# Performance work log

Measured on AMD Instinct MI355X. Metric: run time of the kernel, lower is better.

Reference implementation:

```python
import jax, jax.numpy as jnp
import numpy as np

B, T, N, D = 32, 32, 64, 512
H, OUT = 64, 256


def setup_inputs() -> dict:
    key = jax.random.key(0)
    ks = jax.random.split(key, 7)
    return {
        "inputs": jax.random.normal(ks[0], (B, T, N, D), dtype=jnp.float32),
        "ue_w": jax.random.normal(ks[1], (H, D), dtype=jnp.float32) * (1.0 / np.sqrt(D)),
        "ue_b": jax.random.normal(ks[2], (H,), dtype=jnp.float32) * 0.02,
        "be": jnp.zeros((H,), dtype=jnp.float32),
        "w_w": jax.random.normal(ks[3], (1, H), dtype=jnp.float32) * (1.0 / np.sqrt(H)),
        "w_b": jax.random.normal(ks[4], (1,), dtype=jnp.float32) * 0.02,
        "fc1_w": jax.random.normal(ks[5], (OUT, D), dtype=jnp.float32) * (1.0 / np.sqrt(D)),
        "fc1_b": jax.random.normal(ks[6], (OUT,), dtype=jnp.float32) * 0.02,
    }


def reference(inputs, ue_w, ue_b, be, w_w, w_b, fc1_w, fc1_b):
    # Train path of STAttn.
    b, t, n, d = inputs.shape
    x = inputs.reshape(b * t, n, d)                       # flatten(start=0, end=1)
    h = jnp.einsum('bnd,hd->bnh', x, ue_w) + ue_b + be    # ue(x) + be
    h = jax.nn.leaky_relu(h, negative_slope=0.2)
    e = jnp.einsum('bnh,oh->bno', h, w_w) + w_b           # [BT, N, 1] scores
    a = jax.nn.softmax(e, axis=-2)                        # softmax over N
    attr = jnp.sum(a * x, axis=1)                         # weighted pooling -> [BT, D]
    fc = attr @ fc1_w.T + fc1_b                           # [BT, 256]
    return fc.reshape(b, t, fc.shape[-1]).transpose(1, 0, 2)  # [T, B, 256]
```

## Files before the change

### kernel.cpp

```cpp
#include <hip/hip_runtime.h>


typedef __attribute__((ext_vector_type(8)))  short bf16x8;
typedef __attribute__((ext_vector_type(16))) float f32x16;

#define SPL(f, i) do {                                                        \
    const unsigned u_ = __float_as_uint(f);                                   \
    h8[i] = (short)(u_ >> 16);                                                \
    const float hf_ = __uint_as_float(u_ & 0xFFFF0000u);                      \
    l8[i] = (short)(__float_as_uint((f) - hf_) >> 16);                        \
} while (0)

__device__ __forceinline__ void split8v(float4 va, float4 vb,
                                        bf16x8& h8, bf16x8& l8) {
    SPL(va.x, 0); SPL(va.y, 1); SPL(va.z, 2); SPL(va.w, 3);
    SPL(vb.x, 4); SPL(vb.y, 5); SPL(vb.z, 6); SPL(vb.w, 7);
}

template<int MODE>
__global__ __launch_bounds__(256, 2) void stattn_ea(
    const float* __restrict__ inp,
    const float* __restrict__ ue_w,
    const float* __restrict__ ue_b,
    const float* __restrict__ be,
    const float* __restrict__ w_w,
    const float* __restrict__ fc1_w,
    const float* __restrict__ fc1_b,
    float* __restrict__ dst)
{
    __shared__ float e_s[2][64];
    __shared__ float a_s[2][64];
    __shared__ __align__(16) float attr_s[2][512];

    const int tid = threadIdx.x;
    const int wv  = tid >> 6;
    const int l   = tid & 63;
    const int l31 = l & 31;
    const int hi5 = l >> 5;
    const int g   = wv >> 1;
    const int nh  = wv & 1;
    const long bt = (long)blockIdx.x * 2 + g;
    const float* __restrict__ xg = inp + bt * (64 * 512);

    const float* __restrict__ arow  = xg   + (nh * 32 + l31) * 512 + hi5 * 8;
    const float* __restrict__ brow0 = ue_w + l31 * 512 + hi5 * 8;
    const float* __restrict__ brow1 = brow0 + 32 * 512;

    f32x16 acc0 = {}, acc1 = {};
#pragma unroll 4
    for (int ks = 0; ks < 32; ++ks) {
        const int k = ks * 16;
        const float4 a0  = *reinterpret_cast<const float4*>(&arow[k]);
        const float4 a1  = *reinterpret_cast<const float4*>(&arow[k + 4]);
        const float4 b00 = *reinterpret_cast<const float4*>(&brow0[k]);
        const float4 b01 = *reinterpret_cast<const float4*>(&brow0[k + 4]);
        const float4 b10 = *reinterpret_cast<const float4*>(&brow1[k]);
        const float4 b11 = *reinterpret_cast<const float4*>(&brow1[k + 4]);
        bf16x8 ah, al, bh0, bl0, bh1, bl1;
        { bf16x8 &h8 = ah,  &l8 = al;  split8v(a0,  a1,  h8, l8); }
        { bf16x8 &h8 = bh0, &l8 = bl0; split8v(b00, b01, h8, l8); }
        { bf16x8 &h8 = bh1, &l8 = bl1; split8v(b10, b11, h8, l8); }
        acc0 = __builtin_amdgcn_mfma_f32_32x32x16_bf16(ah, bh0, acc0, 0, 0, 0);
        acc0 = __builtin_amdgcn_mfma_f32_32x32x16_bf16(al, bh0, acc0, 0, 0, 0);
        acc0 = __builtin_amdgcn_mfma_f32_32x32x16_bf16(ah, bl0, acc0, 0, 0, 0);
        acc1 = __builtin_amdgcn_mfma_f32_32x32x16_bf16(ah, bh1, acc1, 0, 0, 0);
        acc1 = __builtin_amdgcn_mfma_f32_32x32x16_bf16(al, bh1, acc1, 0, 0, 0);
        acc1 = __builtin_amdgcn_mfma_f32_32x32x16_bf16(ah, bl1, acc1, 0, 0, 0);
    }

    {
        const int j0 = l31, j1 = l31 + 32;
        const float bias0 = ue_b[j0] + be[j0];
        const float bias1 = ue_b[j1] + be[j1];
        const float ww0 = w_w[j0], ww1 = w_w[j1];
#pragma unroll
        for (int r = 0; r < 16; ++r) {
            float h0 = acc0[r] + bias0; h0 = h0 > 0.f ? h0 : 0.2f * h0;
            float h1 = acc1[r] + bias1; h1 = h1 > 0.f ? h1 : 0.2f * h1;
            float p = h0 * ww0 + h1 * ww1;
            p += __shfl_xor(p, 1);
            p += __shfl_xor(p, 2);
            p += __shfl_xor(p, 4);
            p += __shfl_xor(p, 8);
            p += __shfl_xor(p, 16);
            if (l31 == 0)
                e_s[g][nh * 32 + (r & 3) + 8 * (r >> 2) + 4 * hi5] = p;
        }
    }
    __syncthreads();

    {
        const float v = e_s[g][l];
        float mx = v;
#pragma unroll
        for (int off = 32; off >= 1; off >>= 1) mx = fmaxf(mx, __shfl_xor(mx, off));
        const float ex = expf(v - mx);
        float sm = ex;
#pragma unroll
        for (int off = 32; off >= 1; off >>= 1) sm += __shfl_xor(sm, off);
        a_s[g][l] = ex / sm;
    }
    __syncthreads();

    {
        const float* __restrict__ xp = xg + nh * 256 + 4 * l;
        float sx = 0.f, sy = 0.f, sz = 0.f, sw = 0.f;
#pragma unroll 8
        for (int n = 0; n < 64; ++n) {
            const float an  = a_s[g][n];
            const float4 xv = *reinterpret_cast<const float4*>(&xp[n * 512]);
            sx = fmaf(an, xv.x, sx);
            sy = fmaf(an, xv.y, sy);
            sz = fmaf(an, xv.z, sz);
            sw = fmaf(an, xv.w, sw);
        }
        float4 o; o.x = sx; o.y = sy; o.z = sz; o.w = sw;
        if (MODE == 0) {
            *reinterpret_cast<float4*>(&dst[bt * 512 + nh * 256 + 4 * l]) = o;
        } else {
            *reinterpret_cast<float4*>(&attr_s[g][nh * 256 + 4 * l]) = o;
        }
    }

    if (MODE == 1) {
        __syncthreads();
        const int o = tid;
#pragma unroll
        for (int gg = 0; gg < 2; ++gg) {
            const float* __restrict__ wr = fc1_w + o * 512;
            const float* __restrict__ ap = attr_s[gg];
            float s0 = 0.f, s1 = 0.f, s2 = 0.f, s3 = 0.f;
#pragma unroll 8
            for (int i = 0; i < 128; ++i) {
                const float4 w4 = *reinterpret_cast<const float4*>(&wr[i * 4]);
                const float4 a4 = *reinterpret_cast<const float4*>(&ap[i * 4]);
                s0 = fmaf(a4.x, w4.x, s0);
                s1 = fmaf(a4.y, w4.y, s1);
                s2 = fmaf(a4.z, w4.z, s2);
                s3 = fmaf(a4.w, w4.w, s3);
            }
            const long btg = (long)blockIdx.x * 2 + gg;
            const int row  = (int)(btg & 31) * 32 + (int)(btg >> 5);
            dst[row * 256 + o] = (s0 + s1) + (s2 + s3) + fc1_b[o];
        }
    }
}

__global__ __launch_bounds__(256, 2) void stattn_fc2(
    const float* __restrict__ attr,
    const float* __restrict__ fc1_w,
    const float* __restrict__ fc1_b,
    float* __restrict__ out)
{
    __shared__ __align__(16) float at[32][516];
    const int tid = threadIdx.x;
    const int bm  = blockIdx.x;
    const int bn  = blockIdx.y;

    {
        const int row = tid >> 3;
        const int seg = tid & 7;
        const float* __restrict__ src = attr + (size_t)(bm * 32 + row) * 512 + seg * 64;
#pragma unroll
        for (int q = 0; q < 16; ++q)
            *reinterpret_cast<float4*>(&at[row][seg * 64 + q * 4]) =
                *reinterpret_cast<const float4*>(&src[q * 4]);
    }
    __syncthreads();

    const int tx = tid & 31;
    const int ty = tid >> 5;
    const int o  = bn * 32 + tx;
    const float* __restrict__ wr = fc1_w + (size_t)o * 512;
    float s0 = 0.f, s1 = 0.f, s2 = 0.f, s3 = 0.f;
#pragma unroll 4
    for (int kq = 0; kq < 128; ++kq) {
        const float4 w4 = *reinterpret_cast<const float4*>(&wr[kq * 4]);
        const float4 a0 = *reinterpret_cast<const float4*>(&at[ty * 4 + 0][kq * 4]);
        const float4 a1 = *reinterpret_cast<const float4*>(&at[ty * 4 + 1][kq * 4]);
        const float4 a2 = *reinterpret_cast<const float4*>(&at[ty * 4 + 2][kq * 4]);
        const float4 a3 = *reinterpret_cast<const float4*>(&at[ty * 4 + 3][kq * 4]);
        s0 += a0.x * w4.x + a0.y * w4.y + a0.z * w4.z + a0.w * w4.w;
        s1 += a1.x * w4.x + a1.y * w4.y + a1.z * w4.z + a1.w * w4.w;
        s2 += a2.x * w4.x + a2.y * w4.y + a2.z * w4.z + a2.w * w4.w;
        s3 += a3.x * w4.x + a3.y * w4.y + a3.z * w4.z + a3.w * w4.w;
    }
    const float fb = fc1_b[o];
    float sv0 = s0 + fb, sv1 = s1 + fb, sv2 = s2 + fb, sv3 = s3 + fb;
    {
        int btv = bm * 32 + ty * 4;
        out[((btv & 31) * 32 + (btv >> 5)) * 256 + o] = sv0; ++btv;
        out[((btv & 31) * 32 + (btv >> 5)) * 256 + o] = sv1; ++btv;
        out[((btv & 31) * 32 + (btv >> 5)) * 256 + o] = sv2; ++btv;
        out[((btv & 31) * 32 + (btv >> 5)) * 256 + o] = sv3;
    }
}

extern "C" void kernel_launch(void* const* d_in, const int* in_sizes, int n_in,
                              void* d_out, int out_size, void* d_ws, size_t ws_size,
                              hipStream_t stream) {
    const float* inp   = (const float*)d_in[0];
    const float* ue_w  = (const float*)d_in[1];
    const float* ue_b  = (const float*)d_in[2];
    const float* be    = (const float*)d_in[3];
    const float* w_w   = (const float*)d_in[4];
    const float* fc1_w = (const float*)d_in[6];
    const float* fc1_b = (const float*)d_in[7];
    float* out = (float*)d_out;

    const bool split = ws_size >= (size_t)1024 * 512 * 4;
    if (split) {
        float* attr = (float*)d_ws;
        stattn_ea<0><<<512, 256, 0, stream>>>(inp, ue_w, ue_b, be, w_w,
                                              fc1_w, fc1_b, attr);
        stattn_fc2<<<dim3(32, 8), 256, 0, stream>>>(attr, fc1_w, fc1_b, out);
    } else {
        stattn_ea<1><<<512, 256, 0, stream>>>(inp, ue_w, ue_b, be, w_w,
                                              fc1_w, fc1_b, out);
    }
}
```

Before: 90.58 us.

## Presplit ue weights to bf16 hi/lo and assign one (b,t) per block

```diff
diff --git a/kernel.cpp b/kernel.cpp
--- a/kernel.cpp
+++ b/kernel.cpp
@@ -17,10 +17,34 @@
     SPL(vb.x, 4); SPL(vb.y, 5); SPL(vb.z, 6); SPL(vb.w, 7);
 }
 
-template<int MODE>
-__global__ __launch_bounds__(256, 2) void stattn_ea(
+__global__ __launch_bounds__(256) void presplit_ue(
+    const float* __restrict__ w, unsigned short* __restrict__ hi,
+    unsigned short* __restrict__ lo)
+{
+    const int i4 = (blockIdx.x * 256 + threadIdx.x) * 4;
+    const float4 v = *reinterpret_cast<const float4*>(&w[i4]);
+    ushort4 h, l;
+    {
+        unsigned u;
+        u = __float_as_uint(v.x); h.x = (unsigned short)(u >> 16);
+        l.x = (unsigned short)(__float_as_uint(v.x - __uint_as_float(u & 0xFFFF0000u)) >> 16);
+        u = __float_as_uint(v.y); h.y = (unsigned short)(u >> 16);
+        l.y = (unsigned short)(__float_as_uint(v.y - __uint_as_float(u & 0xFFFF0000u)) >> 16);
+        u = __float_as_uint(v.z); h.z = (unsigned short)(u >> 16);
+        l.z = (unsigned short)(__float_as_uint(v.z - __uint_as_float(u & 0xFFFF0000u)) >> 16);
+        u = __float_as_uint(v.w); h.w = (unsigned short)(u >> 16);
+        l.w = (unsigned short)(__float_as_uint(v.w - __uint_as_float(u & 0xFFFF0000u)) >> 16);
+    }
+    *reinterpret_cast<ushort4*>(&hi[i4]) = h;
+    *reinterpret_cast<ushort4*>(&lo[i4]) = l;
+}
+
+template<int MODE, int PRE>
+__global__ __launch_bounds__(256, 4) void stattn_ea(
     const float* __restrict__ inp,
     const float* __restrict__ ue_w,
+    const unsigned short* __restrict__ ue_hi,
+    const unsigned short* __restrict__ ue_lo,
     const float* __restrict__ ue_b,
     const float* __restrict__ be,
     const float* __restrict__ w_w,
@@ -28,69 +52,80 @@
     const float* __restrict__ fc1_b,
     float* __restrict__ dst)
 {
-    __shared__ float e_s[2][64];
-    __shared__ float a_s[2][64];
-    __shared__ __align__(16) float attr_s[2][512];
+    __shared__ float ep_s[2][64];
+    __shared__ float a_s[64];
+    __shared__ __align__(16) float attr_s[512];
 
     const int tid = threadIdx.x;
     const int wv  = tid >> 6;
     const int l   = tid & 63;
     const int l31 = l & 31;
     const int hi5 = l >> 5;
-    const int g   = wv >> 1;
-    const int nh  = wv & 1;
-    const long bt = (long)blockIdx.x * 2 + g;
-    const float* __restrict__ xg = inp + bt * (64 * 512);
-
-    const float* __restrict__ arow  = xg   + (nh * 32 + l31) * 512 + hi5 * 8;
-    const float* __restrict__ brow0 = ue_w + l31 * 512 + hi5 * 8;
-    const float* __restrict__ brow1 = brow0 + 32 * 512;
-
-    f32x16 acc0 = {}, acc1 = {};
+    const int nh  = wv >> 1;
+    const int jh  = wv & 1;
+    const int bt  = blockIdx.x;
+    const float* __restrict__ xg = inp + (size_t)bt * (64 * 512);
+
+    const float* __restrict__ arow = xg + (nh * 32 + l31) * 512 + hi5 * 8;
+    const int brow = jh * 32 + l31;
+
+    f32x16 acc = {};
+    if (PRE) {
+        const unsigned short* __restrict__ bhp = ue_hi + brow * 512 + hi5 * 8;
+        const unsigned short* __restrict__ blp = ue_lo + brow * 512 + hi5 * 8;
 #pragma unroll 4
-    for (int ks = 0; ks < 32; ++ks) {
-        const int k = ks * 16;
-        const float4 a0  = *reinterpret_cast<const float4*>(&arow[k]);
-        const float4 a1  = *reinterpret_cast<const float4*>(&arow[k + 4]);
-        const float4 b00 = *reinterpret_cast<const float4*>(&brow0[k]);
-        const float4 b01 = *reinterpret_cast<const float4*>(&brow0[k + 4]);
-        const float4 b10 = *reinterpret_cast<const float4*>(&brow1[k]);
-        const float4 b11 = *reinterpret_cast<const float4*>(&brow1[k + 4]);
-        bf16x8 ah, al, bh0, bl0, bh1, bl1;
-        { bf16x8 &h8 = ah,  &l8 = al;  split8v(a0,  a1,  h8, l8); }
-        { bf16x8 &h8 = bh0, &l8 = bl0; split8v(b00, b01, h8, l8); }
-        { bf16x8 &h8 = bh1, &l8 = bl1; split8v(b10, b11, h8, l8); }
-        acc0 = __builtin_amdgcn_mfma_f32_32x32x16_bf16(ah, bh0, acc0, 0, 0, 0);
-        acc0 = __builtin_amdgcn_mfma_f32_32x32x16_bf16(al, bh0, acc0, 0, 0, 0);
-        acc0 = __builtin_amdgcn_mfma_f32_32x32x16_bf16(ah, bl0, acc0, 0, 0, 0);
-        acc1 = __builtin_amdgcn_mfma_f32_32x32x16_bf16(ah, bh1, acc1, 0, 0, 0);
-        acc1 = __builtin_amdgcn_mfma_f32_32x32x16_bf16(al, bh1, acc1, 0, 0, 0);
-        acc1 = __builtin_amdgcn_mfma_f32_32x32x16_bf16(ah, bl1, acc1, 0, 0, 0);
-    }
-
-    {
-        const int j0 = l31, j1 = l31 + 32;
-        const float bias0 = ue_b[j0] + be[j0];
-        const float bias1 = ue_b[j1] + be[j1];
-        const float ww0 = w_w[j0], ww1 = w_w[j1];
+        for (int ks = 0; ks < 32; ++ks) {
+            const int k = ks * 16;
+            const float4 a0 = *reinterpret_cast<const float4*>(&arow[k]);
+            const float4 a1 = *reinterpret_cast<const float4*>(&arow[k + 4]);
+            const bf16x8 bh = *reinterpret_cast<const bf16x8*>(&bhp[k]);
+            const bf16x8 bl = *reinterpret_cast<const bf16x8*>(&blp[k]);
+            bf16x8 h8, l8;
+            split8v(a0, a1, h8, l8);
+            acc = __builtin_amdgcn_mfma_f32_32x32x16_bf16(h8, bh, acc, 0, 0, 0);
+            acc = __builtin_amdgcn_mfma_f32_32x32x16_bf16(l8, bh, acc, 0, 0, 0);
+            acc = __builtin_amdgcn_mfma_f32_32x32x16_bf16(h8, bl, acc, 0, 0, 0);
+        }
+    } else {
+        const float* __restrict__ bp = ue_w + brow * 512 + hi5 * 8;
+#pragma unroll 4
+        for (int ks = 0; ks < 32; ++ks) {
+            const int k = ks * 16;
+            const float4 a0 = *reinterpret_cast<const float4*>(&arow[k]);
+            const float4 a1 = *reinterpret_cast<const float4*>(&arow[k + 4]);
+            const float4 b0 = *reinterpret_cast<const float4*>(&bp[k]);
+            const float4 b1 = *reinterpret_cast<const float4*>(&bp[k + 4]);
+            bf16x8 ah, al, bh, bl;
+            { bf16x8 &h8 = ah, &l8 = al; split8v(a0, a1, h8, l8); }
+            { bf16x8 &h8 = bh, &l8 = bl; split8v(b0, b1, h8, l8); }
+            acc = __builtin_amdgcn_mfma_f32_32x32x16_bf16(ah, bh, acc, 0, 0, 0);
+            acc = __builtin_amdgcn_mfma_f32_32x32x16_bf16(al, bh, acc, 0, 0, 0);
+            acc = __builtin_amdgcn_mfma_f32_32x32x16_bf16(ah, bl, acc, 0, 0, 0);
+        }
+    }
+
+    {
+        const int j = jh * 32 + l31;
+        const float bias = ue_b[j] + be[j];
+        const float ww   = w_w[j];
 #pragma unroll
         for (int r = 0; r < 16; ++r) {
-            float h0 = acc0[r] + bias0; h0 = h0 > 0.f ? h0 : 0.2f * h0;
-            float h1 = acc1[r] + bias1; h1 = h1 > 0.f ? h1 : 0.2f * h1;
-            float p = h0 * ww0 + h1 * ww1;
+            float hv = acc[r] + bias;
+            hv = hv > 0.f ? hv : 0.2f * hv;
+            float p = hv * ww;
             p += __shfl_xor(p, 1);
             p += __shfl_xor(p, 2);
             p += __shfl_xor(p, 4);
             p += __shfl_xor(p, 8);
             p += __shfl_xor(p, 16);
             if (l31 == 0)
-                e_s[g][nh * 32 + (r & 3) + 8 * (r >> 2) + 4 * hi5] = p;
+                ep_s[jh][nh * 32 + (r & 3) + 8 * (r >> 2) + 4 * hi5] = p;
         }
     }
     __syncthreads();
 
-    {
-        const float v = e_s[g][l];
+    if (wv == 0) {
+        const float v = ep_s[0][l] + ep_s[1][l];
         float mx = v;
 #pragma unroll
         for (int off = 32; off >= 1; off >>= 1) mx = fmaxf(mx, __shfl_xor(mx, off));
@@ -98,51 +133,46 @@
         float sm = ex;
 #pragma unroll
         for (int off = 32; off >= 1; off >>= 1) sm += __shfl_xor(sm, off);
-        a_s[g][l] = ex / sm;
+        a_s[l] = ex / sm;
     }
     __syncthreads();
 
     {
-        const float* __restrict__ xp = xg + nh * 256 + 4 * l;
-        float sx = 0.f, sy = 0.f, sz = 0.f, sw = 0.f;
+        const int d0 = tid * 2;
+        const float* __restrict__ xp = xg + d0;
+        float sx = 0.f, sy = 0.f;
 #pragma unroll 8
         for (int n = 0; n < 64; ++n) {
-            const float an  = a_s[g][n];
-            const float4 xv = *reinterpret_cast<const float4*>(&xp[n * 512]);
+            const float an  = a_s[n];
+            const float2 xv = *reinterpret_cast<const float2*>(&xp[n * 512]);
             sx = fmaf(an, xv.x, sx);
             sy = fmaf(an, xv.y, sy);
-            sz = fmaf(an, xv.z, sz);
-            sw = fmaf(an, xv.w, sw);
-        }
-        float4 o; o.x = sx; o.y = sy; o.z = sz; o.w = sw;
+        }
         if (MODE == 0) {
-            *reinterpret_cast<float4*>(&dst[bt * 512 + nh * 256 + 4 * l]) = o;
+            float2 o; o.x = sx; o.y = sy;
+            *reinterpret_cast<float2*>(&dst[(size_t)bt * 512 + d0]) = o;
         } else {
-            *reinterpret_cast<float4*>(&attr_s[g][nh * 256 + 4 * l]) = o;
+            attr_s[d0]     = sx;
+            attr_s[d0 + 1] = sy;
         }
     }
 
     if (MODE == 1) {
         __syncthreads();
         const int o = tid;
-#pragma unroll
-        for (int gg = 0; gg < 2; ++gg) {
-            const float* __restrict__ wr = fc1_w + o * 512;
-            const float* __restrict__ ap = attr_s[gg];
-            float s0 = 0.f, s1 = 0.f, s2 = 0.f, s3 = 0.f;
+        const float* __restrict__ wr = fc1_w + o * 512;
+        float s0 = 0.f, s1 = 0.f, s2 = 0.f, s3 = 0.f;
 #pragma unroll 8
-            for (int i = 0; i < 128; ++i) {
-                const float4 w4 = *reinterpret_cast<const float4*>(&wr[i * 4]);
-                const float4 a4 = *reinterpret_cast<const float4*>(&ap[i * 4]);
-                s0 = fmaf(a4.x, w4.x, s0);
-                s1 = fmaf(a4.y, w4.y, s1);
-                s2 = fmaf(a4.z, w4.z, s2);
-                s3 = fmaf(a4.w, w4.w, s3);
-            }
-            const long btg = (long)blockIdx.x * 2 + gg;
-            const int row  = (int)(btg & 31) * 32 + (int)(btg >> 5);
-            dst[row * 256 + o] = (s0 + s1) + (s2 + s3) + fc1_b[o];
-        }
+        for (int i = 0; i < 128; ++i) {
+            const float4 w4 = *reinterpret_cast<const float4*>(&wr[i * 4]);
+            const float4 a4 = *reinterpret_cast<const float4*>(&attr_s[i * 4]);
+            s0 = fmaf(a4.x, w4.x, s0);
+            s1 = fmaf(a4.y, w4.y, s1);
+            s2 = fmaf(a4.z, w4.z, s2);
+            s3 = fmaf(a4.w, w4.w, s3);
+        }
+        const int row = (bt & 31) * 32 + (bt >> 5);
+        dst[row * 256 + o] = (s0 + s1) + (s2 + s3) + fc1_b[o];
     }
 }
 
@@ -208,14 +238,27 @@
     const float* fc1_b = (const float*)d_in[7];
     float* out = (float*)d_out;
 
-    const bool split = ws_size >= (size_t)1024 * 512 * 4;
+    const size_t ATTR_BYTES = (size_t)1024 * 512 * 4;
+    const size_t PRE_BYTES  = (size_t)64 * 512 * 2 * 2;
+    const bool split = ws_size >= ATTR_BYTES;
+    const bool pre   = ws_size >= ATTR_BYTES + PRE_BYTES;
+
     if (split) {
         float* attr = (float*)d_ws;
-        stattn_ea<0><<<512, 256, 0, stream>>>(inp, ue_w, ue_b, be, w_w,
-                                              fc1_w, fc1_b, attr);
+        unsigned short* ue_hi =
+            (unsigned short*)((char*)d_ws + ATTR_BYTES);
+        unsigned short* ue_lo = ue_hi + 64 * 512;
+        if (pre) {
+            presplit_ue<<<32, 256, 0, stream>>>(ue_w, ue_hi, ue_lo);
+            stattn_ea<0, 1><<<1024, 256, 0, stream>>>(
+                inp, ue_w, ue_hi, ue_lo, ue_b, be, w_w, fc1_w, fc1_b, attr);
+        } else {
+            stattn_ea<0, 0><<<1024, 256, 0, stream>>>(
+                inp, ue_w, ue_hi, ue_lo, ue_b, be, w_w, fc1_w, fc1_b, attr);
+        }
         stattn_fc2<<<dim3(32, 8), 256, 0, stream>>>(attr, fc1_w, fc1_b, out);
     } else {
-        stattn_ea<1><<<512, 256, 0, stream>>>(inp, ue_w, ue_b, be, w_w,
-                                              fc1_w, fc1_b, out);
-    }
-}
+        stattn_ea<1, 0><<<1024, 256, 0, stream>>>(
+            inp, ue_w, nullptr, nullptr, ue_b, be, w_w, fc1_w, fc1_b, out);
+    }
+}
```

After: 107.2 us. +18.3%, slower.
